# Kernel optimization log

Hardware: AMD Instinct MI355X
Metric: run time of the kernel (lower is better)

The kernel has to match this reference:

```python
import jax, jax.numpy as jnp
import numpy as np

DIM = 1024
HEADS = 16
HEAD_DIM = DIM // HEADS
HIDDEN = 4 * DIM
EPS = 1e-5


def _layernorm(x, g, b):
    mu = jnp.mean(x, axis=-1, keepdims=True)
    var = jnp.mean(jnp.square(x - mu), axis=-1, keepdims=True)
    return (x - mu) * jax.lax.rsqrt(var + EPS) * g + b


def setup_inputs() -> dict:
    key = jax.random.key(0)
    ks = jax.random.split(key, 8)
    s = lambda fan_in: 1.0 / np.sqrt(fan_in)
    return {
        "x": jax.random.normal(ks[0], (8, 1024, DIM), dtype=jnp.float32),
        "ln1_g": jnp.ones((DIM,), jnp.float32),
        "ln1_b": jnp.zeros((DIM,), jnp.float32),
        "w_qkv": jax.random.normal(ks[1], (3 * DIM, DIM), jnp.float32) * s(DIM),
        "w_proj": jax.random.normal(ks[2], (DIM, DIM), jnp.float32) * s(DIM),
        "b_proj": jnp.zeros((DIM,), jnp.float32),
        "ln2_g": jnp.ones((DIM,), jnp.float32),
        "ln2_b": jnp.zeros((DIM,), jnp.float32),
        "w_fc1": jax.random.normal(ks[3], (HIDDEN, DIM), jnp.float32) * s(DIM),
        "b_fc1": jnp.zeros((HIDDEN,), jnp.float32),
        "w_fc2": jax.random.normal(ks[4], (DIM, HIDDEN), jnp.float32) * s(HIDDEN),
        "b_fc2": jnp.zeros((DIM,), jnp.float32),
    }


def reference(x, ln1_g, ln1_b, w_qkv, w_proj, b_proj, ln2_g, ln2_b, w_fc1, b_fc1, w_fc2, b_fc2):
    B, N, C = x.shape
    # --- attention branch (pre-norm) ---
    xn = _layernorm(x, ln1_g, ln1_b)
    qkv = xn @ w_qkv.T  # [B,N,3C]
    qkv = qkv.reshape(B, N, 3, HEADS, HEAD_DIM)
    q = qkv[:, :, 0].transpose(0, 2, 1, 3)  # [B,H,N,D]
    k = qkv[:, :, 1].transpose(0, 2, 1, 3)
    v = qkv[:, :, 2].transpose(0, 2, 1, 3)
    scale = HEAD_DIM ** -0.5
    scores = jnp.einsum("bhqd,bhkd->bhqk", q, k) * scale
    attn = jax.nn.softmax(scores, axis=-1)  # [B,H,N,N]
    y = jnp.einsum("bhqk,bhkd->bhqd", attn, v)
    y = y.transpose(0, 2, 1, 3).reshape(B, N, C)
    y = y @ w_proj.T + b_proj
    x = x + y
    # --- MLP branch (pre-norm) ---
    xn2 = _layernorm(x, ln2_g, ln2_b)
    h = jax.nn.gelu(xn2 @ w_fc1.T + b_fc1, approximate=False)
    x = x + (h @ w_fc2.T + b_fc2)
    return (x, attn)
```

## Files before the change

### kernel.cpp

```cpp
#include <hip/hip_runtime.h>
#include <cstdint>
#include <math.h>


typedef _Float16 f16;
typedef _Float16 f16x4 __attribute__((ext_vector_type(4)));
typedef _Float16 f16x8 __attribute__((ext_vector_type(8)));
typedef float f32x4 __attribute__((ext_vector_type(4)));

#define DEV static __device__ __forceinline__

DEV void gload16(const void* g, void* l) {
  __builtin_amdgcn_global_load_lds(
      (__attribute__((address_space(1))) void*)(uintptr_t)g,
      (__attribute__((address_space(3))) void*)(uintptr_t)l, 16, 0, 0);
}

DEV f32x4 mfma16(f16x8 a, f16x8 b, f32x4 c) {
  return __builtin_amdgcn_mfma_f32_16x16x32_f16(a, b, c, 0, 0, 0);
}

DEV float gelu_f(float v) {
  const float a = fabsf(v) * 0.70710678118654752f;
  const float t = 1.0f / (1.0f + 0.3275911f * a);
  const float p = t * (0.254829592f + t * (-0.284496736f + t * (1.421413741f +
                  t * (-1.453152027f + t * 1.061405429f))));
  const float e = p * __expf(-a * a);
  const float erfv = v >= 0.f ? (1.f - e) : (e - 1.f);
  return 0.5f * v * (1.0f + erfv);
}

DEV void nt_core64(const f16* __restrict__ A, const f16* __restrict__ B,
                   size_t lda, size_t ldb, int K, f16* As, f16* Bs,
                   f32x4 acc[4][4])
{
  const int tid  = threadIdx.x;
  const int lane = tid & 63;
  const int w    = tid >> 6;
  const int wm   = (w >> 1) << 6;
  const int wn   = (w & 1) << 6;
  const int frow = lane & 15;
  const int lg   = lane >> 4;

  const int srow0 = w * 32 + (lane >> 3);
  const int scol  = ((lane & 7) ^ ((lane >> 3) & 7)) << 3;
  const f16* Ab = A + (size_t)srow0 * lda + scol;
  const f16* Bb = B + (size_t)srow0 * ldb + scol;
  f16* la = As + w * 2048 + lane * 8;
  f16* lb = Bs + w * 2048 + lane * 8;

  for (int k0 = 0; k0 < K; k0 += 64) {
#pragma unroll
    for (int L = 0; L < 4; ++L)
      gload16(Ab + (size_t)(L * 8) * lda + k0, la + L * 512);
#pragma unroll
    for (int L = 0; L < 4; ++L)
      gload16(Bb + (size_t)(L * 8) * ldb + k0, lb + L * 512);
    __syncthreads();
#pragma unroll
    for (int kc = 0; kc < 2; ++kc) {
      f16x8 af[4], bf[4];
#pragma unroll
      for (int i = 0; i < 4; ++i) {
        const int ra = wm + i * 16 + frow;
        const int rb = wn + i * 16 + frow;
        af[i] = *(const f16x8*)(As + ra * 64 + ((((kc << 2) + lg) ^ (ra & 7)) << 3));
        bf[i] = *(const f16x8*)(Bs + rb * 64 + ((((kc << 2) + lg) ^ (rb & 7)) << 3));
      }
#pragma unroll
      for (int i = 0; i < 4; ++i)
#pragma unroll
        for (int j = 0; j < 4; ++j)
          acc[i][j] = mfma16(af[i], bf[j], acc[i][j]);
    }
    __syncthreads();
  }
}

__global__ __launch_bounds__(256) void k_cvt_ln(const float* __restrict__ s0,
                                                const float* __restrict__ s1,
                                                const float* __restrict__ s2,
                                                const float* __restrict__ s3,
                                                f16* __restrict__ wout,
                                                const float* __restrict__ xin,
                                                const float* __restrict__ g,
                                                const float* __restrict__ bb,
                                                f16* __restrict__ xnout)
{
  __shared__ float red[8];
  const int tid = threadIdx.x;
  if (blockIdx.x < 12288) {
    const int i = blockIdx.x * 256 + tid;
    const float* src;
    int off;
    if (i < 786432)       { src = s0; off = 0; }
    else if (i < 1048576) { src = s1; off = 786432; }
    else if (i < 2097152) { src = s2; off = 1048576; }
    else                  { src = s3; off = 2097152; }
    const float4 f = ((const float4*)src)[i - off];
    f16x4 o; o[0] = (f16)f.x; o[1] = (f16)f.y; o[2] = (f16)f.z; o[3] = (f16)f.w;
    ((f16x4*)wout)[i] = o;
    return;
  }
  const size_t row = blockIdx.x - 12288;
  const float4 v = ((const float4*)(xin + row * 1024))[tid];
  float s  = v.x + v.y + v.z + v.w;
  float sq = v.x * v.x + v.y * v.y + v.z * v.z + v.w * v.w;
#pragma unroll
  for (int off = 32; off > 0; off >>= 1) { s += __shfl_xor(s, off); sq += __shfl_xor(sq, off); }
  if ((tid & 63) == 0) { red[tid >> 6] = s; red[4 + (tid >> 6)] = sq; }
  __syncthreads();
  s  = red[0] + red[1] + red[2] + red[3];
  sq = red[4] + red[5] + red[6] + red[7];
  const float mu = s * (1.0f / 1024.0f);
  const float rs = rsqrtf(sq * (1.0f / 1024.0f) - mu * mu + 1e-5f);
  const float4 gg = ((const float4*)g)[tid];
  const float4 bv = ((const float4*)bb)[tid];
  f16x4 o;
  o[0] = (f16)((v.x - mu) * rs * gg.x + bv.x);
  o[1] = (f16)((v.y - mu) * rs * gg.y + bv.y);
  o[2] = (f16)((v.z - mu) * rs * gg.z + bv.z);
  o[3] = (f16)((v.w - mu) * rs * gg.w + bv.w);
  ((f16x4*)(xnout + row * 1024))[tid] = o;
}

__global__ __launch_bounds__(256) void k_ln(const float* __restrict__ xin,
                                            const float* __restrict__ g,
                                            const float* __restrict__ bb,
                                            f16* __restrict__ out)
{
  __shared__ float red[8];
  const int tid = threadIdx.x;
  const size_t row = blockIdx.x;
  const float4 v = ((const float4*)(xin + row * 1024))[tid];
  float s  = v.x + v.y + v.z + v.w;
  float sq = v.x * v.x + v.y * v.y + v.z * v.z + v.w * v.w;
#pragma unroll
  for (int off = 32; off > 0; off >>= 1) { s += __shfl_xor(s, off); sq += __shfl_xor(sq, off); }
  if ((tid & 63) == 0) { red[tid >> 6] = s; red[4 + (tid >> 6)] = sq; }
  __syncthreads();
  s  = red[0] + red[1] + red[2] + red[3];
  sq = red[4] + red[5] + red[6] + red[7];
  const float mu = s * (1.0f / 1024.0f);
  const float rs = rsqrtf(sq * (1.0f / 1024.0f) - mu * mu + 1e-5f);
  const float4 gg = ((const float4*)g)[tid];
  const float4 bv = ((const float4*)bb)[tid];
  f16x4 o;
  o[0] = (f16)((v.x - mu) * rs * gg.x + bv.x);
  o[1] = (f16)((v.y - mu) * rs * gg.y + bv.y);
  o[2] = (f16)((v.z - mu) * rs * gg.z + bv.z);
  o[3] = (f16)((v.w - mu) * rs * gg.w + bv.w);
  ((f16x4*)(out + row * 1024))[tid] = o;
}

__global__ __launch_bounds__(256) void k_qkv(const f16* __restrict__ xn,
                                             const f16* __restrict__ wq,
                                             f16* __restrict__ qb, f16* __restrict__ kb,
                                             f16* __restrict__ vT)
{
  __shared__ __align__(16) f16 As[8192], Bs[8192];
  f32x4 acc[4][4] = {};
  const int bm = blockIdx.x, bn = blockIdx.y;
  nt_core64(xn + (size_t)bm * 128 * 1024, wq + (size_t)bn * 128 * 1024,
            1024, 1024, 1024, As, Bs, acc);
  const int tid = threadIdx.x, lane = tid & 63, w = tid >> 6;
  const int r0 = bm * 128 + ((w >> 1) << 6) + ((lane >> 4) << 2);
  const int c0 = bn * 128 + ((w & 1) << 6);
  const int sec = (bn * 128) >> 10;
#pragma unroll
  for (int i = 0; i < 4; ++i) {
#pragma unroll
    for (int j = 0; j < 4; ++j) {
      const int o = c0 + j * 16 + (lane & 15);
      const int h = (o & 1023) >> 6, d = o & 63;
#pragma unroll
      for (int e = 0; e < 4; ++e) {
        const int m = r0 + i * 16 + e;
        const int b = m >> 10, n = m & 1023;
        const int bh = (b << 4) + h;
        const f16 val = (f16)acc[i][j][e];
        if (sec == 0)      qb[((size_t)bh * 1024 + n) * 64 + d] = val;
        else if (sec == 1) kb[((size_t)bh * 1024 + n) * 64 + d] = val;
        else               vT[((size_t)bh * 64 + d) * 1024 + n] = val;
      }
    }
  }
}

__global__ __launch_bounds__(256) void k_attn(const f16* __restrict__ qb,
                                              const f16* __restrict__ kb,
                                              const f16* __restrict__ vT,
                                              float* __restrict__ attn,
                                              f16* __restrict__ y2)
{
  __shared__ __align__(16) f16 P[32 * 1024];
  const int tid = threadIdx.x, lane = tid & 63, w = tid >> 6;
  const int lr = lane & 15, lg = lane >> 4;
  const int flat = blockIdx.y * 32 + blockIdx.x;
  const int id2 = (flat & 7) * 512 + (flat >> 3);
  const int bh = id2 >> 5;
  const int m0 = (id2 & 31) * 32;
  const f16* Qb = qb + ((size_t)bh << 16);
  const f16* Kb = kb + ((size_t)bh << 16);
  const f16* Vt = vT + ((size_t)bh << 16);

  f16x8 qf[2][2];
#pragma unroll
  for (int i = 0; i < 2; ++i)
#pragma unroll
    for (int ks = 0; ks < 2; ++ks)
      qf[i][ks] = *(const f16x8*)(Qb + (size_t)(m0 + i * 16 + lr) * 64 + ks * 32 + lg * 8);

  for (int cc = 0; cc < 4; ++cc) {
    const int cb = (w << 8) + (cc << 6);
    f16x8 bf[4][2];
#pragma unroll
    for (int j = 0; j < 4; ++j)
#pragma unroll
      for (int ks = 0; ks < 2; ++ks)
        bf[j][ks] = *(const f16x8*)(Kb + (size_t)(cb + j * 16 + lr) * 64 + ks * 32 + lg * 8);
    f32x4 acc[2][4] = {};
#pragma unroll
    for (int i = 0; i < 2; ++i)
#pragma unroll
      for (int j = 0; j < 4; ++j) {
        acc[i][j] = mfma16(qf[i][0], bf[j][0], acc[i][j]);
        acc[i][j] = mfma16(qf[i][1], bf[j][1], acc[i][j]);
      }
#pragma unroll
    for (int i = 0; i < 2; ++i)
#pragma unroll
      for (int j = 0; j < 4; ++j)
#pragma unroll
        for (int e = 0; e < 4; ++e) {
          const int r = i * 16 + (lg << 2) + e;
          const int c = cb + j * 16 + lr;
          P[(r << 10) + (((c >> 3) ^ (r & 7)) << 3) + (c & 7)] = (f16)(acc[i][j][e] * 0.125f);
        }
  }
  __syncthreads();

  const int r2 = tid >> 3;
  f16* Prow = P + (r2 << 10);
  const int rx = r2 & 7;
  f16x8 vv[16];
  float mrow = -1e30f;
#pragma unroll
  for (int q = 0; q < 16; ++q) {
    const int c = (tid & 7) + (q << 3);
    vv[q] = *(const f16x8*)(Prow + ((c ^ rx) << 3));
#pragma unroll
    for (int e = 0; e < 8; ++e) mrow = fmaxf(mrow, (float)vv[q][e]);
  }
  mrow = fmaxf(mrow, __shfl_xor(mrow, 1));
  mrow = fmaxf(mrow, __shfl_xor(mrow, 2));
  mrow = fmaxf(mrow, __shfl_xor(mrow, 4));
  float ssum = 0.f;
#pragma unroll
  for (int q = 0; q < 16; ++q) {
#pragma unroll
    for (int e = 0; e < 8; ++e) {
      const float ev = __expf((float)vv[q][e] - mrow);
      ssum += ev;
      vv[q][e] = (f16)ev;
    }
  }
  ssum += __shfl_xor(ssum, 1);
  ssum += __shfl_xor(ssum, 2);
  ssum += __shfl_xor(ssum, 4);
  const float inv = 1.0f / ssum;
  float* Aout = attn + ((size_t)bh << 20) + ((size_t)(m0 + r2) << 10);
#pragma unroll
  for (int q = 0; q < 16; ++q) {
    const int c = (tid & 7) + (q << 3);
    f16x8 nv;
    f32x4 o0, o1;
    o0[0] = (float)vv[q][0] * inv; o0[1] = (float)vv[q][1] * inv;
    o0[2] = (float)vv[q][2] * inv; o0[3] = (float)vv[q][3] * inv;
    o1[0] = (float)vv[q][4] * inv; o1[1] = (float)vv[q][5] * inv;
    o1[2] = (float)vv[q][6] * inv; o1[3] = (float)vv[q][7] * inv;
#pragma unroll
    for (int e = 0; e < 8; ++e) nv[e] = (f16)((float)vv[q][e] * inv);
    __builtin_nontemporal_store(o0, (f32x4*)(Aout + (c << 3)));
    __builtin_nontemporal_store(o1, (f32x4*)(Aout + (c << 3)) + 1);
    *(f16x8*)(Prow + ((c ^ rx) << 3)) = nv;
  }
  __syncthreads();

  const int dc = w << 4;
  f32x4 acc2[2] = {};
#pragma unroll 4
  for (int k0 = 0; k0 < 1024; k0 += 32) {
    const f16x8 bf = *(const f16x8*)(Vt + (size_t)(dc + lr) * 1024 + k0 + lg * 8);
#pragma unroll
    for (int i = 0; i < 2; ++i) {
      const int ra = i * 16 + lr;
      const int ch = (k0 >> 3) + lg;
      const f16x8 af = *(const f16x8*)(P + (ra << 10) + ((ch ^ (ra & 7)) << 3));
      acc2[i] = mfma16(af, bf, acc2[i]);
    }
  }
  const int b = bh >> 4, h = bh & 15;
#pragma unroll
  for (int i = 0; i < 2; ++i)
#pragma unroll
    for (int e = 0; e < 4; ++e) {
      const int rloc = i * 16 + (lg << 2) + e;
      y2[(size_t)(b * 1024 + m0 + rloc) * 1024 + (h << 6) + dc + lr] = (f16)acc2[i][e];
    }
}

__global__ __launch_bounds__(256) void k_proj(const f16* __restrict__ y2,
                                              const f16* __restrict__ wp,
                                              const float* __restrict__ bproj,
                                              const float* __restrict__ x,
                                              float* __restrict__ xmid)
{
  __shared__ __align__(16) f16 As[8192], Bs[8192];
  f32x4 acc[4][4] = {};
  nt_core64(y2 + (size_t)blockIdx.x * 128 * 1024, wp + (size_t)blockIdx.y * 128 * 1024,
            1024, 1024, 1024, As, Bs, acc);
  const int tid = threadIdx.x, lane = tid & 63, w = tid >> 6;
  const int r0 = blockIdx.x * 128 + ((w >> 1) << 6) + ((lane >> 4) << 2);
  const int c0 = blockIdx.y * 128 + ((w & 1) << 6) + (lane & 15);
#pragma unroll
  for (int i = 0; i < 4; ++i)
#pragma unroll
    for (int j = 0; j < 4; ++j) {
      const int c = c0 + j * 16;
      const float bias = bproj[c];
#pragma unroll
      for (int e = 0; e < 4; ++e) {
        const size_t idx = (size_t)(r0 + i * 16 + e) * 1024 + c;
        xmid[idx] = acc[i][j][e] + bias + x[idx];
      }
    }
}

__global__ __launch_bounds__(256) void k_fc1(const f16* __restrict__ xn,
                                             const f16* __restrict__ wf,
                                             const float* __restrict__ bfc1,
                                             f16* __restrict__ hb)
{
  __shared__ __align__(16) f16 As[8192], Bs[8192];
  f32x4 acc[4][4] = {};
  nt_core64(xn + (size_t)blockIdx.x * 128 * 1024, wf + (size_t)blockIdx.y * 128 * 1024,
            1024, 1024, 1024, As, Bs, acc);
  const int tid = threadIdx.x, lane = tid & 63, w = tid >> 6;
  const int r0 = blockIdx.x * 128 + ((w >> 1) << 6) + ((lane >> 4) << 2);
  const int c0 = blockIdx.y * 128 + ((w & 1) << 6) + (lane & 15);
#pragma unroll
  for (int i = 0; i < 4; ++i)
#pragma unroll
    for (int j = 0; j < 4; ++j) {
      const int c = c0 + j * 16;
      const float bias = bfc1[c];
#pragma unroll
      for (int e = 0; e < 4; ++e) {
        const float t = acc[i][j][e] + bias;
        hb[(size_t)(r0 + i * 16 + e) * 4096 + c] = (f16)gelu_f(t);
      }
    }
}

__global__ __launch_bounds__(256) void k_fc2(const f16* __restrict__ hb,
                                             const f16* __restrict__ wf,
                                             const float* __restrict__ bfc2,
                                             const float* __restrict__ xmid,
                                             float* __restrict__ out)
{
  __shared__ __align__(16) f16 As[8192], Bs[8192];
  f32x4 acc[4][4] = {};
  nt_core64(hb + (size_t)blockIdx.x * 128 * 4096, wf + (size_t)blockIdx.y * 128 * 4096,
            4096, 4096, 4096, As, Bs, acc);
  const int tid = threadIdx.x, lane = tid & 63, w = tid >> 6;
  const int r0 = blockIdx.x * 128 + ((w >> 1) << 6) + ((lane >> 4) << 2);
  const int c0 = blockIdx.y * 128 + ((w & 1) << 6) + (lane & 15);
#pragma unroll
  for (int i = 0; i < 4; ++i)
#pragma unroll
    for (int j = 0; j < 4; ++j) {
      const int c = c0 + j * 16;
      const float bias = bfc2[c];
#pragma unroll
      for (int e = 0; e < 4; ++e) {
        const size_t idx = (size_t)(r0 + i * 16 + e) * 1024 + c;
        out[idx] = acc[i][j][e] + bias + xmid[idx];
      }
    }
}

extern "C" void kernel_launch(void* const* d_in, const int* in_sizes, int n_in,
                              void* d_out, int out_size, void* d_ws, size_t ws_size,
                              hipStream_t stream)
{
  const float* x     = (const float*)d_in[0];
  const float* ln1g  = (const float*)d_in[1];
  const float* ln1b  = (const float*)d_in[2];
  const float* wqkv  = (const float*)d_in[3];
  const float* wproj = (const float*)d_in[4];
  const float* bproj = (const float*)d_in[5];
  const float* ln2g  = (const float*)d_in[6];
  const float* ln2b  = (const float*)d_in[7];
  const float* wfc1  = (const float*)d_in[8];
  const float* bfc1  = (const float*)d_in[9];
  const float* wfc2  = (const float*)d_in[10];
  const float* bfc2  = (const float*)d_in[11];

  char* ws = (char*)d_ws;
  f16* wqkv_h  = (f16*)(ws);
  f16* wproj_h = (f16*)(ws + 6291456);
  f16* wfc1_h  = (f16*)(ws + 8388608);
  f16* wfc2_h  = (f16*)(ws + 16777216);
  f16* xn      = (f16*)(ws + 25165824);
  f16* qb      = (f16*)(ws + 41943040);
  f16* kb      = (f16*)(ws + 58720256);
  f16* vT      = (f16*)(ws + 75497472);
  f16* y2      = (f16*)(ws + 92274688);
  float* xmid  = (float*)(ws + 109051904);
  f16* hb      = (f16*)(ws + 41943040);

  float* out_x = (float*)d_out;
  float* attn  = (float*)d_out + 8388608;

  k_cvt_ln<<<12288 + 8192, 256, 0, stream>>>(wqkv, wproj, wfc1, wfc2, wqkv_h,
                                             x, ln1g, ln1b, xn);
  k_qkv<<<dim3(64, 24), 256, 0, stream>>>(xn, wqkv_h, qb, kb, vT);
  k_attn<<<dim3(32, 128), 256, 0, stream>>>(qb, kb, vT, attn, y2);
  k_proj<<<dim3(64, 8), 256, 0, stream>>>(y2, wproj_h, bproj, x, xmid);
  k_ln<<<8192, 256, 0, stream>>>(xmid, ln2g, ln2b, xn);
  k_fc1<<<dim3(64, 32), 256, 0, stream>>>(xn, wfc1_h, bfc1, hb);
  k_fc2<<<dim3(64, 8), 256, 0, stream>>>(hb, wfc2_h, bfc2, xmid, out_x);
}
```

Measured before the change: 502.0 us.

## Add 256x256 eight-wave pipelined FC1 GEMM and XCD-aware block swizzle

Replaces the FC1 GEMM with a 512-thread kernel that computes 256x256 output tiles. It double-buffers 128KB of dynamic LDS with async global-to-LDS loads and interleaves four quadrant MFMA phases with explicit barriers, waitcnt and setprio, so loads overlap compute and each tile reuses more data. The QKV, proj and FC2 GEMMs switch to a flat grid with a block remap that groups tiles per XCD for better L2 locality. In exchange, the large LDS footprint limits occupancy to one block per CU, and the hand-tuned waitcnt scheduling is fragile.

```diff
diff --git a/kernel.cpp b/kernel.cpp
--- a/kernel.cpp
+++ b/kernel.cpp
@@ -75,6 +75,147 @@
     }
     __syncthreads();
   }
+}
+
+DEV f16* slotp(f16* L, int buf, int s) { return L + buf * 32768 + s * 8192; }
+
+DEV void stg(const f16* base, int koff, f16* sl, int tid) {
+  gload16(base + koff, sl + tid * 8);
+  gload16(base + koff + (size_t)64 * 1024, sl + 4096 + tid * 8);
+}
+
+DEV void rd_a(const f16* S, int base, int ch0, int ch1, f16x8 af[4][2]) {
+#pragma unroll
+  for (int fi = 0; fi < 4; ++fi) {
+    af[fi][0] = *(const f16x8*)(S + base + fi * 1024 + ch0);
+    af[fi][1] = *(const f16x8*)(S + base + fi * 1024 + ch1);
+  }
+}
+DEV void rd_b(const f16* S, int base, int ch0, int ch1, f16x8 bf[2][2]) {
+#pragma unroll
+  for (int fj = 0; fj < 2; ++fj) {
+    bf[fj][0] = *(const f16x8*)(S + base + fj * 1024 + ch0);
+    bf[fj][1] = *(const f16x8*)(S + base + fj * 1024 + ch1);
+  }
+}
+DEV void mm16(const f16x8 af[4][2], const f16x8 bf[2][2], f32x4 acc[4][2]) {
+  __builtin_amdgcn_s_setprio(1);
+#pragma unroll
+  for (int fi = 0; fi < 4; ++fi)
+#pragma unroll
+    for (int fj = 0; fj < 2; ++fj) {
+      acc[fi][fj] = mfma16(af[fi][0], bf[fj][0], acc[fi][fj]);
+      acc[fi][fj] = mfma16(af[fi][1], bf[fj][1], acc[fi][fj]);
+    }
+  __builtin_amdgcn_s_setprio(0);
+}
+
+#define BAR()  __builtin_amdgcn_s_barrier()
+#define LGKM0() do { asm volatile("s_waitcnt lgkmcnt(0)" ::: "memory"); \
+                     __builtin_amdgcn_sched_barrier(0); } while (0)
+#define VM6()  do { asm volatile("s_waitcnt vmcnt(6)" ::: "memory"); } while (0)
+#define VM0()  do { asm volatile("s_waitcnt vmcnt(0)" ::: "memory"); } while (0)
+#define SCB()  __builtin_amdgcn_sched_barrier(0)
+
+__global__ __launch_bounds__(512) void k_fc18(const f16* __restrict__ xn,
+                                              const f16* __restrict__ wf,
+                                              const float* __restrict__ bfc1,
+                                              f16* __restrict__ hb)
+{
+  extern __shared__ __align__(16) f16 L[];
+  const int flat = blockIdx.x;
+  const int local = flat >> 3;
+  const int bm = (flat & 7) * 4 + (local & 3);
+  const int bn = local >> 2;
+  const int tid = threadIdx.x, lane = tid & 63, w = tid >> 6;
+  const int lr = lane & 15, lg = lane >> 4;
+
+  const int rl = tid >> 3;
+  const int gc = ((tid & 7) ^ (rl & 7)) << 3;
+  const f16* a0 = xn + (size_t)(bm * 256 + rl) * 1024 + gc;
+  const f16* a1 = a0 + (size_t)128 * 1024;
+  const f16* b0 = wf + (size_t)(bn * 256 + rl) * 1024 + gc;
+  const f16* b1 = b0 + (size_t)128 * 1024;
+
+  const int base_ar = ((((w >> 2) << 6) + lr) << 6);
+  const int base_br = ((((w & 3) << 5) + lr) << 6);
+  const int sx = lr & 7;
+  const int ch0 = ((0 + lg) ^ sx) << 3;
+  const int ch1 = ((4 + lg) ^ sx) << 3;
+
+  f32x4 acc0[4][2] = {}, acc1[4][2] = {}, acc2[4][2] = {}, acc3[4][2] = {};
+  f16x8 af[4][2], bfA[2][2], bfB[2][2];
+
+  stg(a0, 0,  slotp(L, 0, 0), tid);
+  stg(b0, 0,  slotp(L, 0, 2), tid);
+  stg(b1, 0,  slotp(L, 0, 3), tid);
+  stg(a1, 0,  slotp(L, 0, 1), tid);
+  stg(a0, 64, slotp(L, 1, 0), tid);
+  stg(b0, 64, slotp(L, 1, 2), tid);
+  asm volatile("s_waitcnt vmcnt(4)" ::: "memory");
+  BAR(); SCB();
+
+  const int NT = 16;
+  for (int t = 0; t < NT; ++t) {
+    const int p = t & 1, nb = p ^ 1;
+    const f16* As0 = slotp(L, p, 0);
+    const f16* As1 = slotp(L, p, 1);
+    const f16* Bs0 = slotp(L, p, 2);
+    const f16* Bs1 = slotp(L, p, 3);
+    const bool s1 = t < NT - 1, s2 = t < NT - 2;
+    const int k1 = (t + 1) * 64, k2 = (t + 2) * 64;
+
+    rd_a(As0, base_ar, ch0, ch1, af);
+    rd_b(Bs0, base_br, ch0, ch1, bfA);
+    if (s1) stg(b1, k1, slotp(L, nb, 3), tid);
+    BAR(); LGKM0();
+    mm16(af, bfA, acc0);
+    if (s2) VM6();
+    BAR(); SCB();
+
+    rd_b(Bs1, base_br, ch0, ch1, bfB);
+    if (s1) stg(a1, k1, slotp(L, nb, 1), tid);
+    BAR(); LGKM0();
+    mm16(af, bfB, acc1);
+    if (s2) VM6();
+    BAR(); SCB();
+
+    rd_a(As1, base_ar, ch0, ch1, af);
+    if (s2) stg(a0, k2, slotp(L, p, 0), tid);
+    BAR(); LGKM0();
+    mm16(af, bfB, acc3);
+    if (s2) VM6();
+    BAR(); SCB();
+
+    if (s2) stg(b0, k2, slotp(L, p, 2), tid);
+    BAR(); SCB();
+    mm16(af, bfA, acc2);
+    if (s2) VM6();
+    else if (s1) VM0();
+    BAR(); SCB();
+  }
+
+  const int r00 = bm * 256 + ((w >> 2) << 6) + (lg << 2);
+  const int c00 = bn * 256 + ((w & 3) << 5) + lr;
+#pragma unroll
+  for (int a = 0; a < 2; ++a)
+#pragma unroll
+    for (int b = 0; b < 2; ++b) {
+      const f32x4 (&A)[4][2] = (a == 0) ? (b == 0 ? acc0 : acc1)
+                                        : (b == 0 ? acc2 : acc3);
+#pragma unroll
+      for (int fj = 0; fj < 2; ++fj) {
+        const int c = c00 + b * 128 + fj * 16;
+        const float bias = bfc1[c];
+#pragma unroll
+        for (int fi = 0; fi < 4; ++fi)
+#pragma unroll
+          for (int e = 0; e < 4; ++e) {
+            const int r = r00 + a * 128 + fi * 16 + e;
+            hb[(size_t)r * 4096 + c] = (f16)gelu_f(A[fi][fj][e] + bias);
+          }
+      }
+    }
 }
 
 __global__ __launch_bounds__(256) void k_cvt_ln(const float* __restrict__ s0,
@@ -160,7 +301,10 @@
 {
   __shared__ __align__(16) f16 As[8192], Bs[8192];
   f32x4 acc[4][4] = {};
-  const int bm = blockIdx.x, bn = blockIdx.y;
+  const int flat = blockIdx.x;
+  const int local = flat >> 3;
+  const int bm = (flat & 7) * 8 + (local & 7);
+  const int bn = local >> 3;
   nt_core64(xn + (size_t)bm * 128 * 1024, wq + (size_t)bn * 128 * 1024,
             1024, 1024, 1024, As, Bs, acc);
   const int tid = threadIdx.x, lane = tid & 63, w = tid >> 6;
@@ -318,11 +462,15 @@
 {
   __shared__ __align__(16) f16 As[8192], Bs[8192];
   f32x4 acc[4][4] = {};
-  nt_core64(y2 + (size_t)blockIdx.x * 128 * 1024, wp + (size_t)blockIdx.y * 128 * 1024,
+  const int flat = blockIdx.x;
+  const int local = flat >> 3;
+  const int bm = (flat & 7) * 8 + (local & 7);
+  const int bn = local >> 3;
+  nt_core64(y2 + (size_t)bm * 128 * 1024, wp + (size_t)bn * 128 * 1024,
             1024, 1024, 1024, As, Bs, acc);
   const int tid = threadIdx.x, lane = tid & 63, w = tid >> 6;
-  const int r0 = blockIdx.x * 128 + ((w >> 1) << 6) + ((lane >> 4) << 2);
-  const int c0 = blockIdx.y * 128 + ((w & 1) << 6) + (lane & 15);
+  const int r0 = bm * 128 + ((w >> 1) << 6) + ((lane >> 4) << 2);
+  const int c0 = bn * 128 + ((w & 1) << 6) + (lane & 15);
 #pragma unroll
   for (int i = 0; i < 4; ++i)
 #pragma unroll
@@ -333,32 +481,6 @@
       for (int e = 0; e < 4; ++e) {
         const size_t idx = (size_t)(r0 + i * 16 + e) * 1024 + c;
         xmid[idx] = acc[i][j][e] + bias + x[idx];
-      }
-    }
-}
-
-__global__ __launch_bounds__(256) void k_fc1(const f16* __restrict__ xn,
-                                             const f16* __restrict__ wf,
-                                             const float* __restrict__ bfc1,
-                                             f16* __restrict__ hb)
-{
-  __shared__ __align__(16) f16 As[8192], Bs[8192];
-  f32x4 acc[4][4] = {};
-  nt_core64(xn + (size_t)blockIdx.x * 128 * 1024, wf + (size_t)blockIdx.y * 128 * 1024,
-            1024, 1024, 1024, As, Bs, acc);
-  const int tid = threadIdx.x, lane = tid & 63, w = tid >> 6;
-  const int r0 = blockIdx.x * 128 + ((w >> 1) << 6) + ((lane >> 4) << 2);
-  const int c0 = blockIdx.y * 128 + ((w & 1) << 6) + (lane & 15);
-#pragma unroll
-  for (int i = 0; i < 4; ++i)
-#pragma unroll
-    for (int j = 0; j < 4; ++j) {
-      const int c = c0 + j * 16;
-      const float bias = bfc1[c];
-#pragma unroll
-      for (int e = 0; e < 4; ++e) {
-        const float t = acc[i][j][e] + bias;
-        hb[(size_t)(r0 + i * 16 + e) * 4096 + c] = (f16)gelu_f(t);
       }
     }
 }
@@ -371,11 +493,15 @@
 {
   __shared__ __align__(16) f16 As[8192], Bs[8192];
   f32x4 acc[4][4] = {};
-  nt_core64(hb + (size_t)blockIdx.x * 128 * 4096, wf + (size_t)blockIdx.y * 128 * 4096,
+  const int flat = blockIdx.x;
+  const int local = flat >> 3;
+  const int bm = (flat & 7) * 8 + (local & 7);
+  const int bn = local >> 3;
+  nt_core64(hb + (size_t)bm * 128 * 4096, wf + (size_t)bn * 128 * 4096,
             4096, 4096, 4096, As, Bs, acc);
   const int tid = threadIdx.x, lane = tid & 63, w = tid >> 6;
-  const int r0 = blockIdx.x * 128 + ((w >> 1) << 6) + ((lane >> 4) << 2);
-  const int c0 = blockIdx.y * 128 + ((w & 1) << 6) + (lane & 15);
+  const int r0 = bm * 128 + ((w >> 1) << 6) + ((lane >> 4) << 2);
+  const int c0 = bn * 128 + ((w & 1) << 6) + (lane & 15);
 #pragma unroll
   for (int i = 0; i < 4; ++i)
 #pragma unroll
@@ -423,12 +549,14 @@
   float* out_x = (float*)d_out;
   float* attn  = (float*)d_out + 8388608;
 
+  hipFuncSetAttribute((const void*)k_fc18, hipFuncAttributeMaxDynamicSharedMemorySize, 131072);
+
   k_cvt_ln<<<12288 + 8192, 256, 0, stream>>>(wqkv, wproj, wfc1, wfc2, wqkv_h,
                                              x, ln1g, ln1b, xn);
-  k_qkv<<<dim3(64, 24), 256, 0, stream>>>(xn, wqkv_h, qb, kb, vT);
+  k_qkv<<<1536, 256, 0, stream>>>(xn, wqkv_h, qb, kb, vT);
   k_attn<<<dim3(32, 128), 256, 0, stream>>>(qb, kb, vT, attn, y2);
-  k_proj<<<dim3(64, 8), 256, 0, stream>>>(y2, wproj_h, bproj, x, xmid);
+  k_proj<<<512, 256, 0, stream>>>(y2, wproj_h, bproj, x, xmid);
   k_ln<<<8192, 256, 0, stream>>>(xmid, ln2g, ln2b, xn);
-  k_fc1<<<dim3(64, 32), 256, 0, stream>>>(xn, wfc1_h, bfc1, hb);
-  k_fc2<<<dim3(64, 8), 256, 0, stream>>>(hb, wfc2_h, bfc2, xmid, out_x);
-}
+  k_fc18<<<512, 512, 131072, stream>>>(xn, wfc1_h, bfc1, hb);
+  k_fc2<<<512, 256, 0, stream>>>(hb, wfc2_h, bfc2, xmid, out_x);
+}
```

Measured after the change: 521.7 us. 1.04x slower.
